# Kernel optimization log

Measured on AMD Instinct MI355X. Metric: run time of the kernel, lower is better.

The kernel has to match this reference:

```python
import jax, jax.numpy as jnp
import numpy as np

HEAD_SIZE = 64
N_EMBED = 768
B, T = 16, 2048


def setup_inputs() -> dict:
    key = jax.random.key(0)
    ks = jax.random.split(key, 7)
    return {
        "x": jax.random.normal(ks[0], (B, T, N_EMBED), dtype=jnp.float32),
        "v1": jax.random.normal(ks[1], (B, T, HEAD_SIZE), dtype=jnp.float32),
        "Wk": jax.random.normal(ks[2], (N_EMBED, HEAD_SIZE), dtype=jnp.float32) * 0.02,
        "Wq": jax.random.normal(ks[3], (N_EMBED, HEAD_SIZE), dtype=jnp.float32) * 0.02,
        "Wv": jax.random.normal(ks[4], (N_EMBED, HEAD_SIZE), dtype=jnp.float32) * 0.02,
        "Wproj": jax.random.normal(ks[5], (HEAD_SIZE, HEAD_SIZE), dtype=jnp.float32) * 0.02,
        "bproj": jnp.zeros((HEAD_SIZE,), dtype=jnp.float32),
        "lamb": jnp.float32(0.5),
    }


def reference(x, v1, Wk, Wq, Wv, Wproj, bproj, lamb):
    # x: [B, T, C]; single-head causal attention with value-residual mixing.
    k = x @ Wk  # [B, T, H]
    q = x @ Wq
    v = x @ Wv
    v = (1.0 - lamb) * v + lamb * v1  # value-residual mix
    scale = jnp.float32(1.0 / np.sqrt(HEAD_SIZE))
    w = jnp.einsum("bth,bsh->bts", q, k) * scale  # [B, T, T]
    t = x.shape[1]
    causal = jnp.tril(jnp.ones((t, t), dtype=bool))  # [T, T]
    w = jnp.where(causal, w, jnp.float32(-jnp.inf))
    w = jax.nn.softmax(w, axis=-1)
    # dropout is identity in eval mode
    out = jnp.einsum("bts,bsh->bth", w, v)  # [B, T, H]
    return out @ Wproj + bproj, v1
```

## Files before the change

### kernel.cpp

```cpp
#include <hip/hip_runtime.h>
#include <hip/hip_bf16.h>


constexpr int BATCH = 16;
constexpr int TSEQ  = 2048;
constexpr int CEMB  = 768;
constexpr int HS    = 64;
constexpr size_t NTOK    = (size_t)BATCH * TSEQ;
constexpr size_t OUTHALF = NTOK * HS;

typedef __bf16 bf16x4 __attribute__((ext_vector_type(4)));
typedef __bf16 bf16x8 __attribute__((ext_vector_type(8)));
typedef float  f32x4  __attribute__((ext_vector_type(4)));

__global__ __launch_bounds__(256) void prep_kernel(
    const float* __restrict__ wk, const float* __restrict__ wq,
    const float* __restrict__ wv, const float* __restrict__ wproj,
    __bf16* __restrict__ wt, __bf16* __restrict__ wpt)
{
    __shared__ __bf16 t[64][66];
    const int bid = blockIdx.x;
    if (bid < 36) {
        const int m = bid / 12, c0 = (bid % 12) * 64;
        const float* src = (m == 0) ? wk : (m == 1) ? wq : wv;
        for (int i = threadIdx.x; i < 4096; i += 256) {
            const int c = i >> 6, h = i & 63;
            t[c][h] = (__bf16)src[(size_t)(c0 + c) * HS + h];
        }
        __syncthreads();
        for (int i = threadIdx.x; i < 4096; i += 256) {
            const int h = i >> 6, c = i & 63;
            wt[(size_t)m * HS * CEMB + (size_t)h * CEMB + c0 + c] = t[c][h];
        }
    } else {
        for (int i = threadIdx.x; i < 4096; i += 256) {
            const int h = i >> 6, hp = i & 63;
            t[h][hp] = (__bf16)wproj[i];
        }
        __syncthreads();
        for (int i = threadIdx.x; i < 4096; i += 256) {
            const int hp = i >> 6, h = i & 63;
            wpt[i] = t[h][hp];
        }
    }
}

__global__ __launch_bounds__(256, 2) void qkv_kernel(
    const float* __restrict__ x,
    const float* __restrict__ v1,
    const __bf16* __restrict__ wt,
    const float* __restrict__ lamb_p,
    __bf16* __restrict__ kk,
    __bf16* __restrict__ qq,
    __bf16* __restrict__ vt)
{
    __shared__ __bf16 xl[2][64][88];

    const int wave = threadIdx.x >> 6;
    const int lane = threadIdx.x & 63;
    const int l16  = lane & 15;
    const int quad = lane >> 4;
    const size_t row0 = (size_t)blockIdx.x * 64;

    const int tok_s = threadIdx.x >> 2;
    const int cq    = threadIdx.x & 3;
    const float* xsrc = x + (row0 + tok_s) * CEMB + cq * 16;

    const __bf16* wbase[3];
    #pragma unroll
    for (int m = 0; m < 3; ++m)
        wbase[m] = wt + ((size_t)m * HS + wave * 16 + l16) * CEMB + quad * 8;

    f32x4 acc[3][4];
    #pragma unroll
    for (int m = 0; m < 3; ++m)
        #pragma unroll
        for (int rt = 0; rt < 4; ++rt)
            acc[m][rt] = (f32x4){0.f, 0.f, 0.f, 0.f};

    {
        f32x4 t0 = *(const f32x4*)(xsrc);
        f32x4 t1 = *(const f32x4*)(xsrc + 4);
        f32x4 t2 = *(const f32x4*)(xsrc + 8);
        f32x4 t3 = *(const f32x4*)(xsrc + 12);
        bf16x8 lo, hi;
        #pragma unroll
        for (int i = 0; i < 4; ++i) {
            lo[i] = (__bf16)t0[i]; lo[i + 4] = (__bf16)t1[i];
            hi[i] = (__bf16)t2[i]; hi[i + 4] = (__bf16)t3[i];
        }
        *(bf16x8*)&xl[0][tok_s][cq * 16]     = lo;
        *(bf16x8*)&xl[0][tok_s][cq * 16 + 8] = hi;
    }
    bf16x8 wc[3][2];
    #pragma unroll
    for (int m = 0; m < 3; ++m)
        #pragma unroll
        for (int ks = 0; ks < 2; ++ks)
            wc[m][ks] = *(const bf16x8*)(wbase[m] + ks * 32);
    __syncthreads();

    for (int c0 = 0; c0 < CEMB; c0 += 64) {
        const int buf = (c0 >> 6) & 1;
        const bool notlast = (c0 + 64 < CEMB);

        f32x4 nx0, nx1, nx2, nx3;
        bf16x8 wn[3][2];
        if (notlast) {
            const float* xs = xsrc + c0 + 64;
            nx0 = *(const f32x4*)(xs);
            nx1 = *(const f32x4*)(xs + 4);
            nx2 = *(const f32x4*)(xs + 8);
            nx3 = *(const f32x4*)(xs + 12);
            #pragma unroll
            for (int m = 0; m < 3; ++m)
                #pragma unroll
                for (int ks = 0; ks < 2; ++ks)
                    wn[m][ks] = *(const bf16x8*)(wbase[m] + c0 + 64 + ks * 32);
        }

        #pragma unroll
        for (int ks = 0; ks < 2; ++ks) {
            bf16x8 a[4];
            #pragma unroll
            for (int rt = 0; rt < 4; ++rt)
                a[rt] = *(const bf16x8*)&xl[buf][rt * 16 + l16][ks * 32 + quad * 8];
            #pragma unroll
            for (int m = 0; m < 3; ++m)
                #pragma unroll
                for (int rt = 0; rt < 4; ++rt)
                    acc[m][rt] = __builtin_amdgcn_mfma_f32_16x16x32_bf16(
                        a[rt], wc[m][ks], acc[m][rt], 0, 0, 0);
        }

        if (notlast) {
            bf16x8 lo, hi;
            #pragma unroll
            for (int i = 0; i < 4; ++i) {
                lo[i] = (__bf16)nx0[i]; lo[i + 4] = (__bf16)nx1[i];
                hi[i] = (__bf16)nx2[i]; hi[i + 4] = (__bf16)nx3[i];
            }
            *(bf16x8*)&xl[buf ^ 1][tok_s][cq * 16]     = lo;
            *(bf16x8*)&xl[buf ^ 1][tok_s][cq * 16 + 8] = hi;
            #pragma unroll
            for (int m = 0; m < 3; ++m)
                #pragma unroll
                for (int ks = 0; ks < 2; ++ks)
                    wc[m][ks] = wn[m][ks];
            __syncthreads();
        }
    }

    const float lam = lamb_p[0];
    const int col = wave * 16 + l16;
    const int b  = (int)(row0 >> 11);
    __bf16* vtb = vt + (size_t)b * HS * TSEQ + (size_t)col * TSEQ;
    #pragma unroll
    for (int rt = 0; rt < 4; ++rt) {
        const size_t tok0 = row0 + rt * 16 + quad * 4;
        bf16x4 pk;
        #pragma unroll
        for (int r = 0; r < 4; ++r) {
            const size_t idx = (tok0 + r) * HS + col;
            kk[idx] = (__bf16)acc[0][rt][r];
            qq[idx] = (__bf16)acc[1][rt][r];
            pk[r] = (__bf16)((1.0f - lam) * acc[2][rt][r] + lam * v1[idx]);
        }
        *(bf16x4*)(vtb + (tok0 & 2047)) = pk;
    }
}

__global__ __launch_bounds__(256, 3) void attn_kernel(
    const __bf16* __restrict__ q,
    const __bf16* __restrict__ k,
    const __bf16* __restrict__ vt,
    const __bf16* __restrict__ wpt,
    const float* __restrict__ bproj,
    float* __restrict__ y)
{
    __shared__ __bf16 plds[4][16][72];
    __shared__ float  mlm[4][16], mll[4][16];

    const int b    = blockIdx.x >> 6;
    const int jp   = blockIdx.x & 63;
    const int wave = threadIdx.x >> 6;
    const int lane = threadIdx.x & 63;
    const int l16  = lane & 15;
    const int quad = lane >> 4;

    const __bf16* kb  = k  + (size_t)b * TSEQ * HS;
    const __bf16* vtb = vt + (size_t)b * HS * TSEQ;
    const float sc2 = 0.125f * 1.44269504f;

    for (int pass = 0; pass < 2; ++pass) {
        const int j = pass ? (127 - jp) : jp;
        const size_t tokbase = (size_t)b * TSEQ + j * 16;
        const int tdiag = j >> 2;

        const __bf16* qbase = q + (tokbase + l16) * HS + quad * 8;
        bf16x8 qf0 = *(const bf16x8*)(qbase);
        bf16x8 qf1 = *(const bf16x8*)(qbase + 32);

        f32x4 o_acc[4];
        #pragma unroll
        for (int nt = 0; nt < 4; ++nt) o_acc[nt] = (f32x4){0.f, 0.f, 0.f, 0.f};
        float m_i[4], l_i[4];
        #pragma unroll
        for (int r = 0; r < 4; ++r) { m_i[r] = -1e30f; l_i[r] = 0.f; }

        bf16x8 kf[8];
        {
            const int s0c = (wave <= tdiag ? wave : tdiag) * 64;
            #pragma unroll
            for (int nt = 0; nt < 4; ++nt) {
                const __bf16* kbp = kb + (size_t)(s0c + nt * 16 + l16) * HS + quad * 8;
                kf[2 * nt]     = *(const bf16x8*)(kbp);
                kf[2 * nt + 1] = *(const bf16x8*)(kbp + 32);
            }
        }

        for (int t = wave; t <= tdiag; t += 4) {
            const int s0 = t * 64;
            f32x4 sc[4];
            #pragma unroll
            for (int nt = 0; nt < 4; ++nt) {
                f32x4 c = (f32x4){0.f, 0.f, 0.f, 0.f};
                c = __builtin_amdgcn_mfma_f32_16x16x32_bf16(qf0, kf[2 * nt], c, 0, 0, 0);
                c = __builtin_amdgcn_mfma_f32_16x16x32_bf16(qf1, kf[2 * nt + 1], c, 0, 0, 0);
                sc[nt] = c;
            }
            {
                const int sn = ((t + 4 <= tdiag) ? (t + 4) : t) * 64;
                #pragma unroll
                for (int nt = 0; nt < 4; ++nt) {
                    const __bf16* kbp = kb + (size_t)(sn + nt * 16 + l16) * HS + quad * 8;
                    kf[2 * nt]     = *(const bf16x8*)(kbp);
                    kf[2 * nt + 1] = *(const bf16x8*)(kbp + 32);
                }
            }
            bf16x8 vf[8];
            #pragma unroll
            for (int ks = 0; ks < 2; ++ks)
                #pragma unroll
                for (int nt = 0; nt < 4; ++nt)
                    vf[ks * 4 + nt] = *(const bf16x8*)(vtb
                        + (size_t)(nt * 16 + l16) * TSEQ + s0 + ks * 32 + quad * 8);

            if (t == tdiag) {
                #pragma unroll
                for (int nt = 0; nt < 4; ++nt)
                    #pragma unroll
                    for (int r = 0; r < 4; ++r) {
                        const int s = s0 + nt * 16 + l16;
                        const int trow = j * 16 + quad * 4 + r;
                        sc[nt][r] = (s <= trow) ? sc[nt][r] * sc2 : -1e30f;
                    }
            } else {
                #pragma unroll
                for (int nt = 0; nt < 4; ++nt)
                    #pragma unroll
                    for (int r = 0; r < 4; ++r) sc[nt][r] *= sc2;
            }

            float mx[4];
            #pragma unroll
            for (int r = 0; r < 4; ++r) {
                mx[r] = fmaxf(fmaxf(sc[0][r], sc[1][r]), fmaxf(sc[2][r], sc[3][r]));
                #pragma unroll
                for (int off = 1; off < 16; off <<= 1)
                    mx[r] = fmaxf(mx[r], __shfl_xor(mx[r], off));
            }
            float alpha[4];
            #pragma unroll
            for (int r = 0; r < 4; ++r) {
                const float mn = fmaxf(m_i[r], mx[r]);
                alpha[r] = exp2f(m_i[r] - mn);
                m_i[r] = mn;
            }
            float rs[4] = {0.f, 0.f, 0.f, 0.f};
            #pragma unroll
            for (int nt = 0; nt < 4; ++nt)
                #pragma unroll
                for (int r = 0; r < 4; ++r) {
                    const float p = exp2f(sc[nt][r] - m_i[r]);
                    rs[r] += p;
                    plds[wave][quad * 4 + r][nt * 16 + l16] = (__bf16)p;
                }
            #pragma unroll
            for (int r = 0; r < 4; ++r) {
                #pragma unroll
                for (int off = 1; off < 16; off <<= 1)
                    rs[r] += __shfl_xor(rs[r], off);
                l_i[r] = l_i[r] * alpha[r] + rs[r];
            }
            #pragma unroll
            for (int nt = 0; nt < 4; ++nt)
                #pragma unroll
                for (int r = 0; r < 4; ++r) o_acc[nt][r] *= alpha[r];

            #pragma unroll
            for (int ks = 0; ks < 2; ++ks) {
                bf16x8 pf = *(const bf16x8*)&plds[wave][l16][ks * 32 + quad * 8];
                #pragma unroll
                for (int nt = 0; nt < 4; ++nt)
                    o_acc[nt] = __builtin_amdgcn_mfma_f32_16x16x32_bf16(
                        pf, vf[ks * 4 + nt], o_acc[nt], 0, 0, 0);
            }
        }

        float invl[4];
        #pragma unroll
        for (int r = 0; r < 4; ++r) invl[r] = (l_i[r] > 0.f) ? 1.0f / l_i[r] : 0.f;
        #pragma unroll
        for (int nt = 0; nt < 4; ++nt)
            #pragma unroll
            for (int r = 0; r < 4; ++r)
                plds[wave][quad * 4 + r][nt * 16 + l16] = (__bf16)(o_acc[nt][r] * invl[r]);
        if (l16 == 0) {
            #pragma unroll
            for (int r = 0; r < 4; ++r) {
                mlm[wave][quad * 4 + r] = m_i[r];
                mll[wave][quad * 4 + r] = l_i[r];
            }
        }
        __syncthreads();

        if (wave == 0) {
            float g[4][4], ginv[4];
            #pragma unroll
            for (int r = 0; r < 4; ++r) {
                const int rw = quad * 4 + r;
                const float ms = fmaxf(fmaxf(mlm[0][rw], mlm[1][rw]),
                                       fmaxf(mlm[2][rw], mlm[3][rw]));
                float gs = 0.f;
                #pragma unroll
                for (int w = 0; w < 4; ++w) {
                    const float gg = exp2f(mlm[w][rw] - ms) * mll[w][rw];
                    g[w][r] = gg;
                    gs += gg;
                }
                ginv[r] = 1.0f / gs;
            }
            float oo[4][4];
            #pragma unroll
            for (int nt = 0; nt < 4; ++nt)
                #pragma unroll
                for (int r = 0; r < 4; ++r) {
                    float o = 0.f;
                    #pragma unroll
                    for (int w = 0; w < 4; ++w)
                        o += g[w][r] * (float)plds[w][quad * 4 + r][nt * 16 + l16];
                    oo[nt][r] = o * ginv[r];
                }
            #pragma unroll
            for (int nt = 0; nt < 4; ++nt)
                #pragma unroll
                for (int r = 0; r < 4; ++r)
                    plds[0][quad * 4 + r][nt * 16 + l16] = (__bf16)oo[nt][r];

            f32x4 res[4];
            #pragma unroll
            for (int nt = 0; nt < 4; ++nt) res[nt] = (f32x4){0.f, 0.f, 0.f, 0.f};
            #pragma unroll
            for (int ks = 0; ks < 2; ++ks) {
                bf16x8 of = *(const bf16x8*)&plds[0][l16][ks * 32 + quad * 8];
                #pragma unroll
                for (int nt = 0; nt < 4; ++nt) {
                    bf16x8 wf = *(const bf16x8*)(wpt + (size_t)(nt * 16 + l16) * HS
                                                 + ks * 32 + quad * 8);
                    res[nt] = __builtin_amdgcn_mfma_f32_16x16x32_bf16(of, wf, res[nt], 0, 0, 0);
                }
            }
            #pragma unroll
            for (int nt = 0; nt < 4; ++nt) {
                const float bp = bproj[nt * 16 + l16];
                #pragma unroll
                for (int r = 0; r < 4; ++r)
                    y[(tokbase + quad * 4 + r) * HS + nt * 16 + l16] = res[nt][r] + bp;
            }
        }
        __syncthreads();
    }
}

__global__ __launch_bounds__(256) void copy_kernel(
    const float* __restrict__ src, float* __restrict__ dst)
{
    const size_t i = ((size_t)blockIdx.x * 256 + threadIdx.x) * 4;
    *(f32x4*)(dst + i) = *(const f32x4*)(src + i);
}

extern "C" void kernel_launch(void* const* d_in, const int* in_sizes, int n_in,
                              void* d_out, int out_size, void* d_ws, size_t ws_size,
                              hipStream_t stream) {
    const float* x     = (const float*)d_in[0];
    const float* v1    = (const float*)d_in[1];
    const float* wk    = (const float*)d_in[2];
    const float* wq    = (const float*)d_in[3];
    const float* wv    = (const float*)d_in[4];
    const float* wproj = (const float*)d_in[5];
    const float* bproj = (const float*)d_in[6];
    const float* lamb  = (const float*)d_in[7];

    float* out = (float*)d_out;
    __bf16* kp  = (__bf16*)(out + OUTHALF);
    __bf16* vtp = kp + OUTHALF;
    __bf16* qp  = (__bf16*)d_ws;
    __bf16* wt  = qp + OUTHALF;
    __bf16* wpt = wt + (size_t)3 * HS * CEMB;

    prep_kernel<<<dim3(37), dim3(256), 0, stream>>>(wk, wq, wv, wproj, wt, wpt);

    qkv_kernel<<<dim3((int)(NTOK / 64)), dim3(256), 0, stream>>>(
        x, v1, wt, lamb, kp, qp, vtp);

    attn_kernel<<<dim3(BATCH * 64), dim3(256), 0, stream>>>(
        qp, kp, vtp, wpt, bproj, out);

    copy_kernel<<<dim3((int)(OUTHALF / (256 * 4))), dim3(256), 0, stream>>>(
        v1, out + OUTHALF);
}
```

Measured before the change: 277.9 us.

## Rewrite attention with 32x32 MFMA tiles, register-resident P, and lazy rescaling

Rewrites the attention kernel so each block handles 32-query tiles using 32x32x16 bf16 MFMAs. S is computed transposed (K×Q), so the P fragment is built in registers with lane shuffles instead of going through LDS. The online softmax skips rescaling unless the running max grows by more than 8. The four per-wave partial outputs are merged in fp32 LDS, and two waves do the output projection with Wproj kept in registers. The grid is halved to 512 blocks with an occupancy hint of 2, which may leave CUs underused and raise register pressure.

```diff
diff --git a/kernel.cpp b/kernel.cpp
--- a/kernel.cpp
+++ b/kernel.cpp
@@ -12,6 +12,8 @@
 typedef __bf16 bf16x4 __attribute__((ext_vector_type(4)));
 typedef __bf16 bf16x8 __attribute__((ext_vector_type(8)));
 typedef float  f32x4  __attribute__((ext_vector_type(4)));
+typedef float  f32x16 __attribute__((ext_vector_type(16)));
+typedef int    i32x4  __attribute__((ext_vector_type(4)));
 
 __global__ __launch_bounds__(256) void prep_kernel(
     const float* __restrict__ wk, const float* __restrict__ wq,
@@ -170,7 +172,25 @@
     }
 }
 
-__global__ __launch_bounds__(256, 3) void attn_kernel(
+__device__ __forceinline__ int pk2(float lo, float hi) {
+    unsigned short a = __builtin_bit_cast(unsigned short, (__bf16)lo);
+    unsigned short b = __builtin_bit_cast(unsigned short, (__bf16)hi);
+    return (int)((((unsigned)b) << 16) | (unsigned)a);
+}
+__device__ __forceinline__ bf16x8 make_bfrag(const float* p, int hi) {
+    const int a0 = pk2(p[0], p[1]), a1 = pk2(p[2], p[3]);
+    const int b0 = pk2(p[4], p[5]), b1 = pk2(p[6], p[7]);
+    const int pa0 = __shfl_xor(a0, 32), pa1 = __shfl_xor(a1, 32);
+    const int pb0 = __shfl_xor(b0, 32), pb1 = __shfl_xor(b1, 32);
+    i32x4 w;
+    w[0] = hi ? pb0 : a0;
+    w[1] = hi ? pb1 : a1;
+    w[2] = hi ? b0  : pa0;
+    w[3] = hi ? b1  : pa1;
+    return __builtin_bit_cast(bf16x8, w);
+}
+
+__global__ __launch_bounds__(256, 2) void attn_kernel(
     const __bf16* __restrict__ q,
     const __bf16* __restrict__ k,
     const __bf16* __restrict__ vt,
@@ -178,205 +198,176 @@
     const float* __restrict__ bproj,
     float* __restrict__ y)
 {
-    __shared__ __bf16 plds[4][16][72];
-    __shared__ float  mlm[4][16], mll[4][16];
-
-    const int b    = blockIdx.x >> 6;
-    const int jp   = blockIdx.x & 63;
+    __shared__ float olds[4][64][32];
+    __shared__ float mred[4][32];
+    __shared__ float lred[4][32];
+
+    const int b    = blockIdx.x >> 5;
+    const int jp   = blockIdx.x & 31;
     const int wave = threadIdx.x >> 6;
     const int lane = threadIdx.x & 63;
-    const int l16  = lane & 15;
-    const int quad = lane >> 4;
-
-    const __bf16* kb  = k  + (size_t)b * TSEQ * HS;
-    const __bf16* vtb = vt + (size_t)b * HS * TSEQ;
+    const int l31  = lane & 31;
+    const int hi   = lane >> 5;
+    const int hi8  = hi * 8;
+
+    const __bf16* kb = k  + (size_t)b * TSEQ * HS;
+    const __bf16* vb = vt + (size_t)b * HS * TSEQ;
     const float sc2 = 0.125f * 1.44269504f;
 
+    bf16x8 wf[4];
+    if (wave < 2) {
+        const __bf16* wp = wpt + (size_t)(wave * 32 + l31) * HS + hi8;
+        #pragma unroll
+        for (int c = 0; c < 4; ++c) wf[c] = *(const bf16x8*)(wp + c * 16);
+    }
+
     for (int pass = 0; pass < 2; ++pass) {
-        const int j = pass ? (127 - jp) : jp;
-        const size_t tokbase = (size_t)b * TSEQ + j * 16;
-        const int tdiag = j >> 2;
-
-        const __bf16* qbase = q + (tokbase + l16) * HS + quad * 8;
-        bf16x8 qf0 = *(const bf16x8*)(qbase);
-        bf16x8 qf1 = *(const bf16x8*)(qbase + 32);
-
-        f32x4 o_acc[4];
-        #pragma unroll
-        for (int nt = 0; nt < 4; ++nt) o_acc[nt] = (f32x4){0.f, 0.f, 0.f, 0.f};
-        float m_i[4], l_i[4];
-        #pragma unroll
-        for (int r = 0; r < 4; ++r) { m_i[r] = -1e30f; l_i[r] = 0.f; }
-
-        bf16x8 kf[8];
-        {
-            const int s0c = (wave <= tdiag ? wave : tdiag) * 64;
-            #pragma unroll
-            for (int nt = 0; nt < 4; ++nt) {
-                const __bf16* kbp = kb + (size_t)(s0c + nt * 16 + l16) * HS + quad * 8;
-                kf[2 * nt]     = *(const bf16x8*)(kbp);
-                kf[2 * nt + 1] = *(const bf16x8*)(kbp + 32);
-            }
-        }
-
-        for (int t = wave; t <= tdiag; t += 4) {
-            const int s0 = t * 64;
-            f32x4 sc[4];
-            #pragma unroll
-            for (int nt = 0; nt < 4; ++nt) {
-                f32x4 c = (f32x4){0.f, 0.f, 0.f, 0.f};
-                c = __builtin_amdgcn_mfma_f32_16x16x32_bf16(qf0, kf[2 * nt], c, 0, 0, 0);
-                c = __builtin_amdgcn_mfma_f32_16x16x32_bf16(qf1, kf[2 * nt + 1], c, 0, 0, 0);
-                sc[nt] = c;
-            }
-            {
-                const int sn = ((t + 4 <= tdiag) ? (t + 4) : t) * 64;
-                #pragma unroll
-                for (int nt = 0; nt < 4; ++nt) {
-                    const __bf16* kbp = kb + (size_t)(sn + nt * 16 + l16) * HS + quad * 8;
-                    kf[2 * nt]     = *(const bf16x8*)(kbp);
-                    kf[2 * nt + 1] = *(const bf16x8*)(kbp + 32);
+        const int j = pass ? (63 - jp) : jp;
+        const size_t tok0 = (size_t)b * TSEQ + (size_t)j * 32;
+
+        const __bf16* qp = q + (tok0 + l31) * HS + hi8;
+        bf16x8 qf[4];
+        #pragma unroll
+        for (int c = 0; c < 4; ++c) qf[c] = *(const bf16x8*)(qp + c * 16);
+
+        f32x16 o0, o1;
+        #pragma unroll
+        for (int r = 0; r < 16; ++r) { o0[r] = 0.f; o1[r] = 0.f; }
+        float m_i = -1e30f, l_i = 0.f;
+
+        bf16x8 kf[4], kn[4];
+        if (wave <= j) {
+            const __bf16* kp = kb + (size_t)(wave * 32 + l31) * HS + hi8;
+            #pragma unroll
+            for (int c = 0; c < 4; ++c) kf[c] = *(const bf16x8*)(kp + c * 16);
+        }
+
+        for (int t = wave; t <= j; t += 4) {
+            const int s0 = t * 32;
+            bf16x8 vf[4];
+            #pragma unroll
+            for (int ht = 0; ht < 2; ++ht)
+                #pragma unroll
+                for (int c2 = 0; c2 < 2; ++c2)
+                    vf[ht * 2 + c2] = *(const bf16x8*)(vb
+                        + (size_t)(ht * 32 + l31) * TSEQ + s0 + c2 * 16 + hi8);
+            if (t + 4 <= j) {
+                const __bf16* kp = kb + (size_t)((t + 4) * 32 + l31) * HS + hi8;
+                #pragma unroll
+                for (int c = 0; c < 4; ++c) kn[c] = *(const bf16x8*)(kp + c * 16);
+            }
+
+            f32x16 s;
+            #pragma unroll
+            for (int r = 0; r < 16; ++r) s[r] = 0.f;
+            #pragma unroll
+            for (int c = 0; c < 4; ++c)
+                s = __builtin_amdgcn_mfma_f32_32x32x16_bf16(kf[c], qf[c], s, 0, 0, 0);
+
+            float p[16];
+            if (t == j) {
+                #pragma unroll
+                for (int r = 0; r < 16; ++r) {
+                    const int krow = (r & 3) + 8 * (r >> 2) + 4 * hi;
+                    p[r] = (krow <= l31) ? s[r] * sc2 : -1e30f;
                 }
-            }
-            bf16x8 vf[8];
-            #pragma unroll
-            for (int ks = 0; ks < 2; ++ks)
-                #pragma unroll
-                for (int nt = 0; nt < 4; ++nt)
-                    vf[ks * 4 + nt] = *(const bf16x8*)(vtb
-                        + (size_t)(nt * 16 + l16) * TSEQ + s0 + ks * 32 + quad * 8);
-
-            if (t == tdiag) {
-                #pragma unroll
-                for (int nt = 0; nt < 4; ++nt)
-                    #pragma unroll
-                    for (int r = 0; r < 4; ++r) {
-                        const int s = s0 + nt * 16 + l16;
-                        const int trow = j * 16 + quad * 4 + r;
-                        sc[nt][r] = (s <= trow) ? sc[nt][r] * sc2 : -1e30f;
-                    }
             } else {
                 #pragma unroll
-                for (int nt = 0; nt < 4; ++nt)
-                    #pragma unroll
-                    for (int r = 0; r < 4; ++r) sc[nt][r] *= sc2;
-            }
-
-            float mx[4];
-            #pragma unroll
-            for (int r = 0; r < 4; ++r) {
-                mx[r] = fmaxf(fmaxf(sc[0][r], sc[1][r]), fmaxf(sc[2][r], sc[3][r]));
-                #pragma unroll
-                for (int off = 1; off < 16; off <<= 1)
-                    mx[r] = fmaxf(mx[r], __shfl_xor(mx[r], off));
-            }
-            float alpha[4];
-            #pragma unroll
-            for (int r = 0; r < 4; ++r) {
-                const float mn = fmaxf(m_i[r], mx[r]);
-                alpha[r] = exp2f(m_i[r] - mn);
-                m_i[r] = mn;
-            }
-            float rs[4] = {0.f, 0.f, 0.f, 0.f};
-            #pragma unroll
-            for (int nt = 0; nt < 4; ++nt)
-                #pragma unroll
-                for (int r = 0; r < 4; ++r) {
-                    const float p = exp2f(sc[nt][r] - m_i[r]);
-                    rs[r] += p;
-                    plds[wave][quad * 4 + r][nt * 16 + l16] = (__bf16)p;
+                for (int r = 0; r < 16; ++r) p[r] = s[r] * sc2;
+            }
+
+            float x0 = fmaxf(p[0], p[1]),   x1 = fmaxf(p[2], p[3]);
+            float x2 = fmaxf(p[4], p[5]),   x3 = fmaxf(p[6], p[7]);
+            float x4 = fmaxf(p[8], p[9]),   x5 = fmaxf(p[10], p[11]);
+            float x6 = fmaxf(p[12], p[13]), x7 = fmaxf(p[14], p[15]);
+            float mx = fmaxf(fmaxf(fmaxf(x0, x1), fmaxf(x2, x3)),
+                             fmaxf(fmaxf(x4, x5), fmaxf(x6, x7)));
+            mx = fmaxf(mx, __shfl_xor(mx, 32));
+
+            if (!__all(mx <= m_i + 8.f)) {
+                const float mn = fmaxf(m_i, mx);
+                const float alpha = exp2f(m_i - mn);
+                m_i = mn;
+                l_i *= alpha;
+                #pragma unroll
+                for (int r = 0; r < 16; ++r) { o0[r] *= alpha; o1[r] *= alpha; }
+            }
+
+            #pragma unroll
+            for (int r = 0; r < 16; ++r) p[r] = exp2f(p[r] - m_i);
+
+            float r0 = (p[0] + p[1]) + (p[2] + p[3]);
+            float r1 = (p[4] + p[5]) + (p[6] + p[7]);
+            float r2 = (p[8] + p[9]) + (p[10] + p[11]);
+            float r3 = (p[12] + p[13]) + (p[14] + p[15]);
+            float rs = (r0 + r1) + (r2 + r3);
+            rs += __shfl_xor(rs, 32);
+            l_i += rs;
+
+            const bf16x8 fb0 = make_bfrag(&p[0], hi);
+            const bf16x8 fb1 = make_bfrag(&p[8], hi);
+
+            o0 = __builtin_amdgcn_mfma_f32_32x32x16_bf16(vf[0], fb0, o0, 0, 0, 0);
+            o0 = __builtin_amdgcn_mfma_f32_32x32x16_bf16(vf[1], fb1, o0, 0, 0, 0);
+            o1 = __builtin_amdgcn_mfma_f32_32x32x16_bf16(vf[2], fb0, o1, 0, 0, 0);
+            o1 = __builtin_amdgcn_mfma_f32_32x32x16_bf16(vf[3], fb1, o1, 0, 0, 0);
+
+            if (t + 4 <= j) {
+                #pragma unroll
+                for (int c = 0; c < 4; ++c) kf[c] = kn[c];
+            }
+        }
+
+        #pragma unroll
+        for (int r = 0; r < 16; ++r) {
+            const int row = (r & 3) + 8 * (r >> 2) + 4 * hi;
+            olds[wave][row][l31]      = o0[r];
+            olds[wave][row + 32][l31] = o1[r];
+        }
+        if (lane < 32) { mred[wave][lane] = m_i; lred[wave][lane] = l_i; }
+        __syncthreads();
+
+        if (wave < 2) {
+            float mw[4], lw[4];
+            #pragma unroll
+            for (int w = 0; w < 4; ++w) { mw[w] = mred[w][l31]; lw[w] = lred[w][l31]; }
+            const float mg = fmaxf(fmaxf(mw[0], mw[1]), fmaxf(mw[2], mw[3]));
+            float g[4], lg = 0.f;
+            #pragma unroll
+            for (int w = 0; w < 4; ++w) { g[w] = exp2f(mw[w] - mg); lg += g[w] * lw[w]; }
+            const float inv = 1.0f / lg;
+
+            float on[32];
+            #pragma unroll
+            for (int r = 0; r < 16; ++r) {
+                const int row = (r & 3) + 8 * (r >> 2) + 4 * hi;
+                float a0 = 0.f, a1 = 0.f;
+                #pragma unroll
+                for (int w = 0; w < 4; ++w) {
+                    a0 += g[w] * olds[w][row][l31];
+                    a1 += g[w] * olds[w][row + 32][l31];
                 }
-            #pragma unroll
-            for (int r = 0; r < 4; ++r) {
-                #pragma unroll
-                for (int off = 1; off < 16; off <<= 1)
-                    rs[r] += __shfl_xor(rs[r], off);
-                l_i[r] = l_i[r] * alpha[r] + rs[r];
-            }
-            #pragma unroll
-            for (int nt = 0; nt < 4; ++nt)
-                #pragma unroll
-                for (int r = 0; r < 4; ++r) o_acc[nt][r] *= alpha[r];
-
-            #pragma unroll
-            for (int ks = 0; ks < 2; ++ks) {
-                bf16x8 pf = *(const bf16x8*)&plds[wave][l16][ks * 32 + quad * 8];
-                #pragma unroll
-                for (int nt = 0; nt < 4; ++nt)
-                    o_acc[nt] = __builtin_amdgcn_mfma_f32_16x16x32_bf16(
-                        pf, vf[ks * 4 + nt], o_acc[nt], 0, 0, 0);
-            }
-        }
-
-        float invl[4];
-        #pragma unroll
-        for (int r = 0; r < 4; ++r) invl[r] = (l_i[r] > 0.f) ? 1.0f / l_i[r] : 0.f;
-        #pragma unroll
-        for (int nt = 0; nt < 4; ++nt)
-            #pragma unroll
-            for (int r = 0; r < 4; ++r)
-                plds[wave][quad * 4 + r][nt * 16 + l16] = (__bf16)(o_acc[nt][r] * invl[r]);
-        if (l16 == 0) {
-            #pragma unroll
-            for (int r = 0; r < 4; ++r) {
-                mlm[wave][quad * 4 + r] = m_i[r];
-                mll[wave][quad * 4 + r] = l_i[r];
-            }
-        }
-        __syncthreads();
-
-        if (wave == 0) {
-            float g[4][4], ginv[4];
-            #pragma unroll
-            for (int r = 0; r < 4; ++r) {
-                const int rw = quad * 4 + r;
-                const float ms = fmaxf(fmaxf(mlm[0][rw], mlm[1][rw]),
-                                       fmaxf(mlm[2][rw], mlm[3][rw]));
-                float gs = 0.f;
-                #pragma unroll
-                for (int w = 0; w < 4; ++w) {
-                    const float gg = exp2f(mlm[w][rw] - ms) * mll[w][rw];
-                    g[w][r] = gg;
-                    gs += gg;
-                }
-                ginv[r] = 1.0f / gs;
-            }
-            float oo[4][4];
-            #pragma unroll
-            for (int nt = 0; nt < 4; ++nt)
-                #pragma unroll
-                for (int r = 0; r < 4; ++r) {
-                    float o = 0.f;
-                    #pragma unroll
-                    for (int w = 0; w < 4; ++w)
-                        o += g[w][r] * (float)plds[w][quad * 4 + r][nt * 16 + l16];
-                    oo[nt][r] = o * ginv[r];
-                }
-            #pragma unroll
-            for (int nt = 0; nt < 4; ++nt)
-                #pragma unroll
-                for (int r = 0; r < 4; ++r)
-                    plds[0][quad * 4 + r][nt * 16 + l16] = (__bf16)oo[nt][r];
-
-            f32x4 res[4];
-            #pragma unroll
-            for (int nt = 0; nt < 4; ++nt) res[nt] = (f32x4){0.f, 0.f, 0.f, 0.f};
-            #pragma unroll
-            for (int ks = 0; ks < 2; ++ks) {
-                bf16x8 of = *(const bf16x8*)&plds[0][l16][ks * 32 + quad * 8];
-                #pragma unroll
-                for (int nt = 0; nt < 4; ++nt) {
-                    bf16x8 wf = *(const bf16x8*)(wpt + (size_t)(nt * 16 + l16) * HS
-                                                 + ks * 32 + quad * 8);
-                    res[nt] = __builtin_amdgcn_mfma_f32_16x16x32_bf16(of, wf, res[nt], 0, 0, 0);
-                }
-            }
-            #pragma unroll
-            for (int nt = 0; nt < 4; ++nt) {
-                const float bp = bproj[nt * 16 + l16];
-                #pragma unroll
-                for (int r = 0; r < 4; ++r)
-                    y[(tokbase + quad * 4 + r) * HS + nt * 16 + l16] = res[nt][r] + bp;
+                on[r]      = a0 * inv;
+                on[r + 16] = a1 * inv;
+            }
+
+            f32x16 res;
+            #pragma unroll
+            for (int r = 0; r < 16; ++r) res[r] = 0.f;
+            #pragma unroll
+            for (int c = 0; c < 4; ++c) {
+                const bf16x8 ob = make_bfrag(&on[c * 8], hi);
+                res = __builtin_amdgcn_mfma_f32_32x32x16_bf16(wf[c], ob, res, 0, 0, 0);
+            }
+
+            float* yp = y + (tok0 + l31) * HS + wave * 32;
+            #pragma unroll
+            for (int grp = 0; grp < 4; ++grp) {
+                const f32x4 bb = *(const f32x4*)(bproj + wave * 32 + grp * 8 + 4 * hi);
+                f32x4 o4;
+                #pragma unroll
+                for (int rr = 0; rr < 4; ++rr) o4[rr] = res[grp * 4 + rr] + bb[rr];
+                *(f32x4*)(yp + grp * 8 + 4 * hi) = o4;
             }
         }
         __syncthreads();
@@ -414,7 +405,7 @@
     qkv_kernel<<<dim3((int)(NTOK / 64)), dim3(256), 0, stream>>>(
         x, v1, wt, lamb, kp, qp, vtp);
 
-    attn_kernel<<<dim3(BATCH * 64), dim3(256), 0, stream>>>(
+    attn_kernel<<<dim3(BATCH * 32), dim3(256), 0, stream>>>(
         qp, kp, vtp, wpt, bproj, out);
 
     copy_kernel<<<dim3((int)(OUTHALF / (256 * 4))), dim3(256), 0, stream>>>(
```

Result: faster. 229.7 us (-17.4%).
